# Kernel tuning notes

Hardware: AMD Instinct MI355X
Metric: run time of the kernel (lower is better)

The kernel has to match this reference:

```python
import jax, jax.numpy as jnp
import numpy as np

VOCAB = 50257
D = 1024
EDGES = [0, 20000, 40000, VOCAB]  # cluster boundaries
HSZ = [1024, 256, 64]             # D // 4**i per cluster


def setup_inputs() -> dict:
    key = jax.random.key(0)
    ks = jax.random.split(key, 8)
    emb_input = jax.random.randint(ks[0], (8, 2048), 0, VOCAB, dtype=jnp.int64)
    inp = {"emb_input": emb_input}
    for i in range(3):
        vsz = EDGES[i + 1] - EDGES[i]
        h = HSZ[i]
        inp[f"emb{i}"] = jax.random.normal(ks[1 + 2 * i], (vsz, h), dtype=jnp.float32) * 0.02
        # nn.Linear(h, D, bias=False) weight has shape [D, h]
        inp[f"w{i}"] = jax.random.normal(ks[2 + 2 * i], (D, h), dtype=jnp.float32) * 0.02
    return inp


def reference(emb_input, emb0, w0, emb1, w1, emb2, w2):
    B, S = emb_input.shape
    idx = emb_input.reshape(-1)  # [N]
    clusters = [(emb0, w0), (emb1, w1), (emb2, w2)]
    out = jnp.zeros((idx.shape[0], D), dtype=jnp.float32)
    for i, (emb, w) in enumerate(clusters):
        lo, hi = EDGES[i], EDGES[i + 1]
        mask = (idx >= lo) & (idx < hi)                       # [N]
        local = jnp.clip(idx - lo, 0, emb.shape[0] - 1)       # in-range gather ids
        h = emb[local]                                        # [N, hsz_i]
        proj = jnp.einsum('nh,dh->nd', h, w)                  # [N, D]
        out = out + jnp.where(mask[:, None], proj, 0.0)
    return out.reshape(B, S, D)
```

## Files before the change

### kernel.cpp

```cpp
#include <hip/hip_runtime.h>
#include <hip/hip_bf16.h>
#include <stdint.h>

#define DOUT 1024
#define NMAX 16384

typedef __attribute__((ext_vector_type(8))) short short8;
typedef __attribute__((ext_vector_type(4))) float floatx4;

__device__ __forceinline__ unsigned short f2bf(float f) {
  union { float f; uint32_t u; } v;
  v.f = f;
  return (unsigned short)((v.u + 0x7FFFu + ((v.u >> 16) & 1u)) >> 16);
}

__device__ __forceinline__ short8 cvt8(float4 a, float4 b) {
  __hip_bfloat162 p0 = __float22bfloat162_rn(make_float2(a.x, a.y));
  __hip_bfloat162 p1 = __float22bfloat162_rn(make_float2(a.z, a.w));
  __hip_bfloat162 p2 = __float22bfloat162_rn(make_float2(b.x, b.y));
  __hip_bfloat162 p3 = __float22bfloat162_rn(make_float2(b.z, b.w));
  union { __hip_bfloat162 h[4]; short8 s; } u;
  u.h[0] = p0; u.h[1] = p1; u.h[2] = p2; u.h[3] = p3;
  return u.s;
}

__global__ __launch_bounds__(256) void classify_cvt_kernel(
    const int* __restrict__ idx, int* __restrict__ cnt,
    int* __restrict__ bucket, int* __restrict__ blocal, int N,
    const float* __restrict__ w0, const float* __restrict__ w1,
    const float* __restrict__ w2, unsigned short* __restrict__ wb0,
    unsigned short* __restrict__ wb1, unsigned short* __restrict__ wb2) {
  if (blockIdx.x < 64) {
    int n = blockIdx.x * 256 + threadIdx.x;
    int lane = threadIdx.x & 63;
    int c = -1, v = 0;
    if (n < N) {
      v = idx[n];
      c = (v < 20000) ? 0 : ((v < 40000) ? 1 : 2);
    }
#pragma unroll
    for (int k = 0; k < 3; ++k) {
      unsigned long long m = __ballot(c == k);
      if (c == k) {
        int leader = __ffsll((unsigned long long)m) - 1;
        int base = 0;
        if (lane == leader) base = atomicAdd(&cnt[k], (int)__popcll(m));
        base = __shfl(base, leader);
        int rank = (int)__popcll(m & ((1ull << (unsigned)lane) - 1ull));
        int lo = (k == 0) ? 0 : (k == 1) ? 20000 : 40000;
        bucket[k * NMAX + base + rank] = n;
        blocal[k * NMAX + base + rank] = v - lo;
      }
    }
  } else {
    int i = (blockIdx.x - 64) * 256 + threadIdx.x;
    if (i >= 344064) return;
    const float4* src;
    ushort4* dst;
    if (i < 262144) {
      src = (const float4*)w0 + i;
      dst = (ushort4*)wb0 + i;
    } else if (i < 327680) {
      src = (const float4*)w1 + (i - 262144);
      dst = (ushort4*)wb1 + (i - 262144);
    } else {
      src = (const float4*)w2 + (i - 327680);
      dst = (ushort4*)wb2 + (i - 327680);
    }
    float4 v = *src;
    ushort4 o;
    o.x = f2bf(v.x); o.y = f2bf(v.y); o.z = f2bf(v.z); o.w = f2bf(v.w);
    *dst = o;
  }
}

template <int H>
__device__ __forceinline__ void gemm_body(
    const float* __restrict__ emb, const unsigned short* __restrict__ B,
    int count, const int* __restrict__ bucket, const int* __restrict__ blocal,
    float* __restrict__ out, unsigned short* As, unsigned short* Bs,
    int* rowTok, int* rowLoc) {
  const int m0 = blockIdx.y * 64;
  if (m0 >= count) return;
  const int n0 = blockIdx.x * 128;

  const int tid = threadIdx.x;
  const int wave = tid >> 6;
  const int lane = tid & 63;
  const int quad = lane >> 4;
  const int l16 = lane & 15;
  const int wm = wave & 1;
  const int wn = wave >> 1;

  if (tid < 64) {
    int m = m0 + tid;
    rowTok[tid] = (m < count) ? bucket[m] : -1;
    rowLoc[tid] = (m < count) ? blocal[m] : 0;
  }
  __syncthreads();

  floatx4 acc[2][4];
#pragma unroll
  for (int i = 0; i < 2; ++i)
#pragma unroll
    for (int j = 0; j < 4; ++j) acc[i][j] = (floatx4){0.f, 0.f, 0.f, 0.f};

  const char* Bb = (const char*)B;
  const int row_lo = tid >> 2;
  const int ck = tid & 3;

  const float* arow = emb + (size_t)rowLoc[row_lo] * H + ck * 8;

  for (int k0 = 0; k0 < H; k0 += 64) {
    __syncthreads();
#pragma unroll
    for (int t = 0; t < 2; ++t) {
      const float* src = arow + k0 + t * 32;
      float4 v0 = *(const float4*)src;
      float4 v1 = *(const float4*)(src + 4);
      *(short8*)&As[t * 2048 + row_lo * 32 + ck * 8] = cvt8(v0, v1);
    }
#pragma unroll
    for (int t = 0; t < 2; ++t)
#pragma unroll
      for (int p = 0; p < 2; ++p) {
        const void* gb =
            Bb + ((size_t)(n0 + p * 64 + row_lo) * H + k0 + t * 32) * 2 + ck * 16;
        void* lb = (char*)Bs + (t * 8192 + p * 4096 + wave * 1024);
        __builtin_amdgcn_global_load_lds(
            (const __attribute__((address_space(1))) void*)gb,
            (__attribute__((address_space(3))) void*)lb, 16, 0, 0);
      }
    __syncthreads();

#pragma unroll
    for (int t = 0; t < 2; ++t) {
      short8 af[2], bf[4];
#pragma unroll
      for (int mi = 0; mi < 2; ++mi)
        af[mi] = *(const short8*)&As[t * 2048 + (wm * 32 + mi * 16 + l16) * 32 + quad * 8];
#pragma unroll
      for (int ni = 0; ni < 4; ++ni)
        bf[ni] = *(const short8*)&Bs[t * 4096 + (wn * 64 + ni * 16 + l16) * 32 + quad * 8];
#pragma unroll
      for (int mi = 0; mi < 2; ++mi)
#pragma unroll
        for (int ni = 0; ni < 4; ++ni)
          acc[mi][ni] = __builtin_amdgcn_mfma_f32_16x16x32_bf16(
              af[mi], bf[ni], acc[mi][ni], 0, 0, 0);
    }
  }

  const int colBase = n0 + wn * 64 + l16;
#pragma unroll
  for (int mi = 0; mi < 2; ++mi) {
#pragma unroll
    for (int r = 0; r < 4; ++r) {
      int tok = rowTok[wm * 32 + mi * 16 + quad * 4 + r];
      if (tok >= 0) {
        float* o = out + (size_t)tok * DOUT + colBase;
#pragma unroll
        for (int ni = 0; ni < 4; ++ni) o[ni * 16] = acc[mi][ni][r];
      }
    }
  }
}

__global__ __launch_bounds__(256) void gemm_fused(
    const float* __restrict__ emb0, const float* __restrict__ emb1,
    const float* __restrict__ emb2, const unsigned short* __restrict__ wb0,
    const unsigned short* __restrict__ wb1, const unsigned short* __restrict__ wb2,
    const int* __restrict__ cnt, const int* __restrict__ bucket,
    const int* __restrict__ blocal, float* __restrict__ out) {
  __shared__ __align__(16) unsigned short As[2 * 64 * 32];
  __shared__ __align__(16) unsigned short Bs[2 * 128 * 32];
  __shared__ int rowTok[64];
  __shared__ int rowLoc[64];

  const int z = blockIdx.z;
  if (z == 0)
    gemm_body<1024>(emb0, wb0, cnt[0], bucket + 0 * NMAX, blocal + 0 * NMAX,
                    out, As, Bs, rowTok, rowLoc);
  else if (z == 1)
    gemm_body<256>(emb1, wb1, cnt[1], bucket + 1 * NMAX, blocal + 1 * NMAX,
                   out, As, Bs, rowTok, rowLoc);
  else
    gemm_body<64>(emb2, wb2, cnt[2], bucket + 2 * NMAX, blocal + 2 * NMAX,
                  out, As, Bs, rowTok, rowLoc);
}

extern "C" void kernel_launch(void* const* d_in, const int* in_sizes, int n_in,
                              void* d_out, int out_size, void* d_ws, size_t ws_size,
                              hipStream_t stream) {
  const int* idx = (const int*)d_in[0];
  const float* emb0 = (const float*)d_in[1];
  const float* w0 = (const float*)d_in[2];
  const float* emb1 = (const float*)d_in[3];
  const float* w1 = (const float*)d_in[4];
  const float* emb2 = (const float*)d_in[5];
  const float* w2 = (const float*)d_in[6];
  float* out = (float*)d_out;
  const int N = in_sizes[0];

  char* ws = (char*)d_ws;
  int* cnt = (int*)ws;
  int* bucket = (int*)(ws + 1024);
  int* blocal = bucket + 3 * NMAX;
  size_t off = 1024 + (size_t)6 * NMAX * 4;
  off = (off + 255) & ~(size_t)255;
  unsigned short* wb0 = (unsigned short*)(ws + off); off += (size_t)DOUT * 1024 * 2;
  unsigned short* wb1 = (unsigned short*)(ws + off); off += (size_t)DOUT * 256 * 2;
  unsigned short* wb2 = (unsigned short*)(ws + off); off += (size_t)DOUT * 64 * 2;

  hipMemsetAsync(cnt, 0, 16 * sizeof(int), stream);

  classify_cvt_kernel<<<64 + 1344, 256, 0, stream>>>(
      idx, cnt, bucket, blocal, N, w0, w1, w2, wb0, wb1, wb2);

  dim3 grid(DOUT / 128, NMAX / 64, 3);
  gemm_fused<<<grid, 256, 0, stream>>>(emb0, emb1, emb2, wb0, wb1, wb2,
                                       cnt, bucket, blocal, out);
}
```

Baseline: 208.9 us.

## Pre-gather embeddings to packed bf16 buffer and enlarge GEMM M tile

```diff
diff --git a/kernel.cpp b/kernel.cpp
--- a/kernel.cpp
+++ b/kernel.cpp
@@ -74,13 +74,46 @@
   }
 }
 
+__global__ __launch_bounds__(256) void gather_kernel(
+    const float* __restrict__ emb0, const float* __restrict__ emb1,
+    const float* __restrict__ emb2, const int* __restrict__ cnt,
+    const int* __restrict__ blocal, unsigned short* __restrict__ Abf) {
+  const int b = blockIdx.x;
+  const int c0 = cnt[0], c1 = cnt[1], c2 = cnt[2];
+  const float* emb;
+  const int* bl;
+  int H, count, baseRow, lg;
+  size_t off;
+  if (b < 4096) {
+    emb = emb0; bl = blocal; H = 1024; count = c0; off = 0;
+    baseRow = b * 4; lg = 6;
+  } else if (b < 5120) {
+    emb = emb1; bl = blocal + NMAX; H = 256; count = c1;
+    off = (size_t)c0 * 1024; baseRow = (b - 4096) * 16; lg = 4;
+  } else {
+    emb = emb2; bl = blocal + 2 * NMAX; H = 64; count = c2;
+    off = (size_t)c0 * 1024 + (size_t)c1 * 256; baseRow = (b - 5120) * 64; lg = 2;
+  }
+  const int tid = threadIdx.x;
+  const int r = baseRow + (tid >> lg);
+  if (r >= count) return;
+  const int e = (tid & ((1 << lg) - 1)) * 16;
+  const float* src = emb + (size_t)bl[r] * H + e;
+  unsigned short* d = Abf + off + (size_t)r * H + e;
+  float4 v0 = ((const float4*)src)[0];
+  float4 v1 = ((const float4*)src)[1];
+  float4 v2 = ((const float4*)src)[2];
+  float4 v3 = ((const float4*)src)[3];
+  *(short8*)d = cvt8(v0, v1);
+  *(short8*)(d + 8) = cvt8(v2, v3);
+}
+
 template <int H>
 __device__ __forceinline__ void gemm_body(
-    const float* __restrict__ emb, const unsigned short* __restrict__ B,
-    int count, const int* __restrict__ bucket, const int* __restrict__ blocal,
-    float* __restrict__ out, unsigned short* As, unsigned short* Bs,
-    int* rowTok, int* rowLoc) {
-  const int m0 = blockIdx.y * 64;
+    const unsigned short* __restrict__ A, const unsigned short* __restrict__ B,
+    int count, const int* __restrict__ bucket, float* __restrict__ out,
+    unsigned short* As, unsigned short* Bs, int* rowTok) {
+  const int m0 = blockIdx.y * 128;
   if (m0 >= count) return;
   const int n0 = blockIdx.x * 128;
 
@@ -92,40 +125,36 @@
   const int wm = wave & 1;
   const int wn = wave >> 1;
 
-  if (tid < 64) {
+  if (tid < 128) {
     int m = m0 + tid;
     rowTok[tid] = (m < count) ? bucket[m] : -1;
-    rowLoc[tid] = (m < count) ? blocal[m] : 0;
-  }
-  __syncthreads();
-
-  floatx4 acc[2][4];
-#pragma unroll
-  for (int i = 0; i < 2; ++i)
+  }
+
+  floatx4 acc[4][4];
+#pragma unroll
+  for (int i = 0; i < 4; ++i)
 #pragma unroll
     for (int j = 0; j < 4; ++j) acc[i][j] = (floatx4){0.f, 0.f, 0.f, 0.f};
 
+  const char* Ab = (const char*)A;
   const char* Bb = (const char*)B;
-  const int row_lo = tid >> 2;
+  const int row = tid >> 2;
   const int ck = tid & 3;
-
-  const float* arow = emb + (size_t)rowLoc[row_lo] * H + ck * 8;
 
   for (int k0 = 0; k0 < H; k0 += 64) {
     __syncthreads();
 #pragma unroll
-    for (int t = 0; t < 2; ++t) {
-      const float* src = arow + k0 + t * 32;
-      float4 v0 = *(const float4*)src;
-      float4 v1 = *(const float4*)(src + 4);
-      *(short8*)&As[t * 2048 + row_lo * 32 + ck * 8] = cvt8(v0, v1);
-    }
-#pragma unroll
     for (int t = 0; t < 2; ++t)
 #pragma unroll
       for (int p = 0; p < 2; ++p) {
+        const void* ga =
+            Ab + ((size_t)(m0 + p * 64 + row) * H + k0 + t * 32) * 2 + ck * 16;
+        void* la = (char*)As + (t * 8192 + p * 4096 + wave * 1024);
+        __builtin_amdgcn_global_load_lds(
+            (const __attribute__((address_space(1))) void*)ga,
+            (__attribute__((address_space(3))) void*)la, 16, 0, 0);
         const void* gb =
-            Bb + ((size_t)(n0 + p * 64 + row_lo) * H + k0 + t * 32) * 2 + ck * 16;
+            Bb + ((size_t)(n0 + p * 64 + row) * H + k0 + t * 32) * 2 + ck * 16;
         void* lb = (char*)Bs + (t * 8192 + p * 4096 + wave * 1024);
         __builtin_amdgcn_global_load_lds(
             (const __attribute__((address_space(1))) void*)gb,
@@ -135,15 +164,15 @@
 
 #pragma unroll
     for (int t = 0; t < 2; ++t) {
-      short8 af[2], bf[4];
-#pragma unroll
-      for (int mi = 0; mi < 2; ++mi)
-        af[mi] = *(const short8*)&As[t * 2048 + (wm * 32 + mi * 16 + l16) * 32 + quad * 8];
+      short8 af[4], bf[4];
+#pragma unroll
+      for (int mi = 0; mi < 4; ++mi)
+        af[mi] = *(const short8*)&As[t * 4096 + (wm * 64 + mi * 16 + l16) * 32 + quad * 8];
 #pragma unroll
       for (int ni = 0; ni < 4; ++ni)
         bf[ni] = *(const short8*)&Bs[t * 4096 + (wn * 64 + ni * 16 + l16) * 32 + quad * 8];
 #pragma unroll
-      for (int mi = 0; mi < 2; ++mi)
+      for (int mi = 0; mi < 4; ++mi)
 #pragma unroll
         for (int ni = 0; ni < 4; ++ni)
           acc[mi][ni] = __builtin_amdgcn_mfma_f32_16x16x32_bf16(
@@ -153,10 +182,10 @@
 
   const int colBase = n0 + wn * 64 + l16;
 #pragma unroll
-  for (int mi = 0; mi < 2; ++mi) {
+  for (int mi = 0; mi < 4; ++mi) {
 #pragma unroll
     for (int r = 0; r < 4; ++r) {
-      int tok = rowTok[wm * 32 + mi * 16 + quad * 4 + r];
+      int tok = rowTok[wm * 64 + mi * 16 + quad * 4 + r];
       if (tok >= 0) {
         float* o = out + (size_t)tok * DOUT + colBase;
 #pragma unroll
@@ -166,27 +195,27 @@
   }
 }
 
-__global__ __launch_bounds__(256) void gemm_fused(
-    const float* __restrict__ emb0, const float* __restrict__ emb1,
-    const float* __restrict__ emb2, const unsigned short* __restrict__ wb0,
-    const unsigned short* __restrict__ wb1, const unsigned short* __restrict__ wb2,
-    const int* __restrict__ cnt, const int* __restrict__ bucket,
-    const int* __restrict__ blocal, float* __restrict__ out) {
-  __shared__ __align__(16) unsigned short As[2 * 64 * 32];
+__global__ __launch_bounds__(256) void gemm_bucketed(
+    const unsigned short* __restrict__ Abf,
+    const unsigned short* __restrict__ wb0,
+    const unsigned short* __restrict__ wb1,
+    const unsigned short* __restrict__ wb2, const int* __restrict__ cnt,
+    const int* __restrict__ bucket, float* __restrict__ out) {
+  __shared__ __align__(16) unsigned short As[2 * 128 * 32];
   __shared__ __align__(16) unsigned short Bs[2 * 128 * 32];
-  __shared__ int rowTok[64];
-  __shared__ int rowLoc[64];
+  __shared__ int rowTok[128];
 
   const int z = blockIdx.z;
+  const int c0 = cnt[0];
+  const int c1 = cnt[1];
   if (z == 0)
-    gemm_body<1024>(emb0, wb0, cnt[0], bucket + 0 * NMAX, blocal + 0 * NMAX,
-                    out, As, Bs, rowTok, rowLoc);
+    gemm_body<1024>(Abf, wb0, c0, bucket, out, As, Bs, rowTok);
   else if (z == 1)
-    gemm_body<256>(emb1, wb1, cnt[1], bucket + 1 * NMAX, blocal + 1 * NMAX,
-                   out, As, Bs, rowTok, rowLoc);
+    gemm_body<256>(Abf + (size_t)c0 * 1024, wb1, c1, bucket + NMAX, out, As,
+                   Bs, rowTok);
   else
-    gemm_body<64>(emb2, wb2, cnt[2], bucket + 2 * NMAX, blocal + 2 * NMAX,
-                  out, As, Bs, rowTok, rowLoc);
+    gemm_body<64>(Abf + (size_t)c0 * 1024 + (size_t)c1 * 256, wb2, cnt[2],
+                  bucket + 2 * NMAX, out, As, Bs, rowTok);
 }
 
 extern "C" void kernel_launch(void* const* d_in, const int* in_sizes, int n_in,
@@ -211,13 +240,17 @@
   unsigned short* wb0 = (unsigned short*)(ws + off); off += (size_t)DOUT * 1024 * 2;
   unsigned short* wb1 = (unsigned short*)(ws + off); off += (size_t)DOUT * 256 * 2;
   unsigned short* wb2 = (unsigned short*)(ws + off); off += (size_t)DOUT * 64 * 2;
+  off = (off + 255) & ~(size_t)255;
+  unsigned short* Abf = (unsigned short*)(ws + off);
+  off += (size_t)(NMAX + 128) * 1024 * 2;
 
   hipMemsetAsync(cnt, 0, 16 * sizeof(int), stream);
 
   classify_cvt_kernel<<<64 + 1344, 256, 0, stream>>>(
       idx, cnt, bucket, blocal, N, w0, w1, w2, wb0, wb1, wb2);
 
-  dim3 grid(DOUT / 128, NMAX / 64, 3);
-  gemm_fused<<<grid, 256, 0, stream>>>(emb0, emb1, emb2, wb0, wb1, wb2,
-                                       cnt, bucket, blocal, out);
-}
+  gather_kernel<<<5376, 256, 0, stream>>>(emb0, emb1, emb2, cnt, blocal, Abf);
+
+  dim3 grid(DOUT / 128, NMAX / 128, 3);
+  gemm_bucketed<<<grid, 256, 0, stream>>>(Abf, wb0, wb1, wb2, cnt, bucket, out);
+}
```

Result: faster. 198.4 us (-5.0%).
